# Optimization experiments

Measured on AMD Instinct MI355X. Metric: run time of the kernel, lower is better.

## Reference

```python
import jax, jax.numpy as jnp
import numpy as np

B, S, D, H = 4, 2048, 512, 4
HD = D // H
EPS = 1e-5


def layer_norm(x, gamma, beta):
    mu = jnp.mean(x, axis=-1, keepdims=True)
    var = jnp.mean(jnp.square(x - mu), axis=-1, keepdims=True)
    return (x - mu) * jax.lax.rsqrt(var + EPS) * gamma + beta


def setup_inputs() -> dict:
    key = jax.random.key(0)
    ks = jax.random.split(key, 16)
    s_in = 1.0 / np.sqrt(D)
    s_ex = 1.0 / np.sqrt(2 * D)
    return {
        "input_states": jax.random.normal(ks[0], (B, S, D), jnp.float32),
        "positions": jax.random.normal(ks[1], (B, S, 3), jnp.float32),
        "W_expand": jax.random.uniform(ks[2], (D, 2 * D), jnp.float32, -s_in, s_in),
        "b_expand": jax.random.uniform(ks[3], (2 * D,), jnp.float32, -s_in, s_in),
        "W_squeeze": jax.random.uniform(ks[4], (2 * D, D), jnp.float32, -s_ex, s_ex),
        "b_squeeze": jax.random.uniform(ks[5], (D,), jnp.float32, -s_ex, s_ex),
        "gamma": jnp.ones((D,), jnp.float32),
        "beta": jnp.zeros((D,), jnp.float32),
        "Wq": jax.random.uniform(ks[6], (D, D), jnp.float32, -s_in, s_in),
        "bq": jax.random.uniform(ks[7], (D,), jnp.float32, -s_in, s_in),
        "Wk": jax.random.uniform(ks[8], (D, D), jnp.float32, -s_in, s_in),
        "bk": jax.random.uniform(ks[9], (D,), jnp.float32, -s_in, s_in),
        "Wv": jax.random.uniform(ks[10], (D, D), jnp.float32, -s_in, s_in),
        "bv": jax.random.uniform(ks[11], (D,), jnp.float32, -s_in, s_in),
        "alpha": jnp.float32(0.1),
    }


def reference(input_states, positions, W_expand, b_expand, W_squeeze, b_squeeze,
              gamma, beta, Wq, bq, Wk, bk, Wv, bv, alpha):
    # FFN (expand -> relu -> squeeze) + residual + LayerNorm
    h = jax.nn.relu(input_states @ W_expand + b_expand)
    squeezed = h @ W_squeeze + b_squeeze
    se = layer_norm(input_states + squeezed, gamma, beta)

    # q/k/v projections, split heads: [B,H,S,HD]
    q = (se @ Wq + bq).reshape(B, S, H, HD).transpose(0, 2, 1, 3)
    k = (se @ Wk + bk).reshape(B, S, H, HD).transpose(0, 2, 1, 3)
    v = (se @ Wv + bv).reshape(B, S, H, HD).transpose(0, 2, 1, 3)

    scores = jnp.einsum('bhid,bhjd->bhij', q, k) / np.sqrt(HD)

    # squared pairwise distance bias: ||pi||^2 + ||pj||^2 - 2 pi.pj, broadcast over heads
    sq = jnp.sum(positions * positions, axis=-1)  # [B,S]
    dist2 = sq[:, :, None] + sq[:, None, :] - 2.0 * jnp.einsum('bic,bjc->bij', positions, positions)
    dist2 = jnp.maximum(dist2, 0.0)
    scores = scores - alpha * dist2[:, None, :, :]

    w = jax.nn.softmax(scores, axis=-1)
    ctx = jnp.einsum('bhij,bhjd->bhid', w, v)
    ctx = ctx.transpose(0, 2, 1, 3).reshape(B, S, D)

    # same LayerNorm params reused (self.norm applied twice in original)
    return layer_norm(se + ctx, gamma, beta)
```

## Files before the change

kernel.cpp:

```cpp
#include <hip/hip_runtime.h>

typedef __bf16 bf16_t;
typedef __attribute__((ext_vector_type(8))) __bf16 bf16x8;
typedef __attribute__((ext_vector_type(4))) __bf16 bf16x4;
typedef __attribute__((ext_vector_type(4))) float f32x4;

constexpr int Bc = 4, Sc = 2048, Dc = 512, Hc = 4, HDc = 128;
constexpr int Mrows = Bc * Sc;

__device__ inline void gl2lds(const void* g, void* l) {
  __builtin_amdgcn_global_load_lds(
      (__attribute__((address_space(1))) void*)g,
      (__attribute__((address_space(3))) void*)l, 16, 0, 0);
}

__global__ __launch_bounds__(256) void wt_transpose_k(const float* __restrict__ src,
                                                      bf16_t* __restrict__ dst,
                                                      int K, int N) {
  __shared__ float tile[32][33];
  const int tx = threadIdx.x & 31, ty = threadIdx.x >> 5;
  const int n0 = blockIdx.x * 32, k0 = blockIdx.y * 32;
#pragma unroll
  for (int i = 0; i < 4; i++)
    tile[ty + i * 8][tx] = src[(long)(k0 + ty + i * 8) * N + n0 + tx];
  __syncthreads();
#pragma unroll
  for (int i = 0; i < 4; i++)
    dst[(long)(n0 + ty + i * 8) * K + k0 + tx] = (bf16_t)tile[tx][ty + i * 8];
}

__global__ __launch_bounds__(256) void cvt_k(const float* __restrict__ x,
                                             bf16_t* __restrict__ y) {
  const long i = ((long)blockIdx.x * 256 + threadIdx.x) * 8;
  const float4 a = *(const float4*)(x + i);
  const float4 c = *(const float4*)(x + i + 4);
  bf16x8 o;
  o[0] = (bf16_t)a.x; o[1] = (bf16_t)a.y; o[2] = (bf16_t)a.z; o[3] = (bf16_t)a.w;
  o[4] = (bf16_t)c.x; o[5] = (bf16_t)c.y; o[6] = (bf16_t)c.z; o[7] = (bf16_t)c.w;
  *(bf16x8*)(y + i) = o;
}

__global__ __launch_bounds__(256) void pospack_k(const float* __restrict__ pos,
                                                 float* __restrict__ pos2) {
  const int i = blockIdx.x * 256 + threadIdx.x;
  const float x = pos[(long)i * 3], y = pos[(long)i * 3 + 1], z = pos[(long)i * 3 + 2];
  float4 o; o.x = x; o.y = y; o.z = z; o.w = 0.f;
  *(float4*)(pos2 + (long)i * 4) = o;
}

template <int OMODE>
__global__ __launch_bounds__(256, 2) void gemm128_k(
    const bf16_t* __restrict__ A, const bf16_t* __restrict__ Bt,
    const float* __restrict__ bias0, const float* __restrict__ bias1,
    const float* __restrict__ bias2, void* __restrict__ out0,
    void* __restrict__ out1, void* __restrict__ out2, int N, int K) {
  __shared__ bf16_t As[128 * 32];
  __shared__ bf16_t Bs[128 * 32];
  const int t = threadIdx.x;
  const int n0 = blockIdx.x * 128, m0 = blockIdx.y * 128;
  const int lane = t & 63, wave = t >> 6;
  const int quad = lane >> 4, ln = lane & 15;
  const int wm = wave >> 1, wn = wave & 1;
  const int srow = wave * 16 + (lane >> 2);
  const int scol = (lane & 3) * 8;
  const bf16_t* aseg = A + (long)(m0 + srow) * K + scol;
  const bf16_t* bseg = Bt + (long)(n0 + srow) * K + scol;
  bf16_t* asl = &As[(wave * 16) * 32];
  bf16_t* bsl = &Bs[(wave * 16) * 32];
  f32x4 acc[4][4] = {};
  for (int k0 = 0; k0 < K; k0 += 32) {
#pragma unroll
    for (int i = 0; i < 2; i++) {
      gl2lds(aseg + (long)i * 64 * K + k0, asl + i * 64 * 32);
      gl2lds(bseg + (long)i * 64 * K + k0, bsl + i * 64 * 32);
    }
    __syncthreads();
    bf16x8 af[4], bfr[4];
#pragma unroll
    for (int mt = 0; mt < 4; mt++)
      af[mt] = *(const bf16x8*)&As[(wm * 64 + mt * 16 + ln) * 32 + quad * 8];
#pragma unroll
    for (int nt = 0; nt < 4; nt++)
      bfr[nt] = *(const bf16x8*)&Bs[(wn * 64 + nt * 16 + ln) * 32 + quad * 8];
#pragma unroll
    for (int mt = 0; mt < 4; mt++)
#pragma unroll
      for (int nt = 0; nt < 4; nt++)
        acc[mt][nt] = __builtin_amdgcn_mfma_f32_16x16x32_bf16(af[mt], bfr[nt],
                                                              acc[mt][nt], 0, 0, 0);
    __syncthreads();
  }
#pragma unroll
  for (int nt = 0; nt < 4; nt++) {
    const int gcol = n0 + wn * 64 + nt * 16 + ln;
    if constexpr (OMODE == 0 || OMODE == 1) {
      const float bv = bias0[gcol];
      bf16_t* o = (bf16_t*)out0;
#pragma unroll
      for (int mt = 0; mt < 4; mt++)
#pragma unroll
        for (int r = 0; r < 4; r++) {
          const int grow = m0 + wm * 64 + mt * 16 + quad * 4 + r;
          float vv = acc[mt][nt][r] + bv;
          if constexpr (OMODE == 0) vv = vv > 0.f ? vv : 0.f;
          o[(long)grow * N + gcol] = (bf16_t)vv;
        }
    } else {
      const int which = gcol >> 9, n = gcol & 511;
      const int hh = n >> 7, hd = n & 127;
      const float bv = (which == 0 ? bias0 : which == 1 ? bias1 : bias2)[n];
      bf16_t* o = (bf16_t*)(which == 0 ? out0 : which == 1 ? out1 : out2);
#pragma unroll
      for (int mt = 0; mt < 4; mt++)
#pragma unroll
        for (int r = 0; r < 4; r++) {
          const int grow = m0 + wm * 64 + mt * 16 + quad * 4 + r;
          const int b = grow >> 11, s = grow & 2047;
          const float vv = acc[mt][nt][r] + bv;
          long idx;
          if (which == 2)
            idx = ((long)(b * Hc + hh) * HDc + hd) * Sc + s;
          else
            idx = ((long)(b * Hc + hh) * Sc + s) * HDc + hd;
          o[idx] = (bf16_t)vv;
        }
    }
  }
}

template <int DUAL>
__global__ __launch_bounds__(256) void ln_k(const float* __restrict__ xa,
                                            const bf16_t* __restrict__ xb,
                                            const float* __restrict__ gamma,
                                            const float* __restrict__ beta,
                                            float* __restrict__ out,
                                            bf16_t* __restrict__ outb) {
  const int wave = threadIdx.x >> 6, lane = threadIdx.x & 63;
  const long row = (long)blockIdx.x * 4 + wave;
  const float* a = xa + row * Dc;
  const bf16_t* bp = xb + row * Dc;
  float vv[8];
  float s = 0.f, s2 = 0.f;
#pragma unroll
  for (int i = 0; i < 2; i++) {
    const float4 va = *(const float4*)(a + lane * 4 + i * 256);
    const bf16x4 vb = *(const bf16x4*)(bp + lane * 4 + i * 256);
    const float xs[4] = {va.x, va.y, va.z, va.w};
#pragma unroll
    for (int j = 0; j < 4; j++) {
      const float x = xs[j] + (float)vb[j];
      vv[i * 4 + j] = x;
      s += x;
      s2 += x * x;
    }
  }
#pragma unroll
  for (int off = 1; off < 64; off <<= 1) {
    s += __shfl_xor(s, off, 64);
    s2 += __shfl_xor(s2, off, 64);
  }
  const float mu = s * (1.f / Dc);
  const float var = s2 * (1.f / Dc) - mu * mu;
  const float rstd = rsqrtf(var + 1e-5f);
#pragma unroll
  for (int i = 0; i < 2; i++)
#pragma unroll
    for (int j = 0; j < 4; j++) {
      const int col = lane * 4 + i * 256 + j;
      const float o = (vv[i * 4 + j] - mu) * rstd * gamma[col] + beta[col];
      out[row * Dc + col] = o;
      if constexpr (DUAL) outb[row * Dc + col] = (bf16_t)o;
    }
}

__global__ __launch_bounds__(256, 2) void attn_k(const bf16_t* __restrict__ q,
                                                 const bf16_t* __restrict__ k,
                                                 const bf16_t* __restrict__ v,
                                                 const float* __restrict__ pos2,
                                                 const float* __restrict__ alphap,
                                                 bf16_t* __restrict__ ctx) {
  __shared__ bf16_t Ks[2][64 * 128];
  __shared__ bf16_t Vts[2][128 * 64];
  __shared__ float pk[2][64][4];
  __shared__ bf16_t Ps[4][16][72];
  const int t = threadIdx.x;
  const int qt = blockIdx.x, h = blockIdx.y, b = blockIdx.z;
  const int q0 = qt * 64;
  const int wave = t >> 6, lane = t & 63, quad = lane >> 4, ln = lane & 15;
  const int ln7 = ln & 7;
  const float l2e = 1.4426950408889634f;
  const float scale_l2 = 0.08838834764831845f * l2e;
  const float alpha_l2 = alphap[0] * l2e;
  const bf16_t* kbase = k + (long)(b * Hc + h) * Sc * HDc;
  const bf16_t* vbase = v + (long)(b * Hc + h) * HDc * Sc;

  bf16x8 qf[4];
#pragma unroll
  for (int kc = 0; kc < 4; kc++)
    qf[kc] = *(const bf16x8*)(q + ((long)(b * Hc + h) * Sc + q0 + wave * 16 + ln) * HDc +
                              kc * 32 + quad * 8);
  float pqx[4], pqy[4], pqz[4];
#pragma unroll
  for (int r = 0; r < 4; r++) {
    const float4 p = *(const float4*)(pos2 + ((long)b * Sc + q0 + wave * 16 + quad * 4 + r) * 4);
    pqx[r] = p.x; pqy[r] = p.y; pqz[r] = p.z;
  }

  const int krw = wave * 16 + (lane >> 4);
  const int kg = lane & 15;
  const int vrw = wave * 32 + (lane >> 3);
  const int vg = lane & 7;
  auto stage = [&](int buf, int kt) {
#pragma unroll
    for (int i = 0; i < 4; i++) {
      const int row = krw + i * 4;
      gl2lds(kbase + (long)(kt * 64 + row) * HDc + (kg ^ (row & 7)) * 8,
             &Ks[buf][wave * 2048 + i * 512]);
    }
#pragma unroll
    for (int i = 0; i < 4; i++) {
      const int row = vrw + i * 8;
      gl2lds(vbase + (long)row * Sc + kt * 64 + (vg ^ (row & 7)) * 8,
             &Vts[buf][wave * 2048 + i * 512]);
    }
    if (wave == 0)
      gl2lds(pos2 + ((long)b * Sc + kt * 64) * 4, &pk[buf][0][0]);
  };
  stage(0, 0);

  float rs[4] = {0.f, 0.f, 0.f, 0.f};
  f32x4 acc_o[8] = {};

  for (int kt = 0; kt < Sc / 64; kt++) {
    const int cur = kt & 1;
    __syncthreads();
    if (kt < Sc / 64 - 1) stage(1 - cur, kt + 1);

    f32x4 sacc[4] = {};
#pragma unroll
    for (int kc = 0; kc < 4; kc++)
#pragma unroll
      for (int ct = 0; ct < 4; ct++) {
        const bf16x8 bfv = *(const bf16x8*)&Ks[cur][(ct * 16 + ln) * 128 +
                                                    ((kc * 4 + quad) ^ ln7) * 8];
        sacc[ct] = __builtin_amdgcn_mfma_f32_16x16x32_bf16(qf[kc], bfv, sacc[ct], 0, 0, 0);
      }
#pragma unroll
    for (int ct = 0; ct < 4; ct++) {
      const int kk = ct * 16 + ln;
      const float4 pkv = *(const float4*)&pk[cur][kk][0];
#pragma unroll
      for (int r = 0; r < 4; r++) {
        const float dx = pqx[r] - pkv.x, dy = pqy[r] - pkv.y, dz = pqz[r] - pkv.z;
        const float d2 = dx * dx + dy * dy + dz * dz;
        const float p = __builtin_amdgcn_exp2f(sacc[ct][r] * scale_l2 - alpha_l2 * d2);
        rs[r] += p;
        Ps[wave][quad * 4 + r][kk] = (bf16_t)p;
      }
    }
#pragma unroll
    for (int s2 = 0; s2 < 2; s2++) {
      const bf16x8 pf = *(const bf16x8*)&Ps[wave][ln][s2 * 32 + quad * 8];
#pragma unroll
      for (int nt = 0; nt < 8; nt++) {
        const bf16x8 vf = *(const bf16x8*)&Vts[cur][(nt * 16 + ln) * 64 +
                                                    ((s2 * 4 + quad) ^ ln7) * 8];
        acc_o[nt] = __builtin_amdgcn_mfma_f32_16x16x32_bf16(pf, vf, acc_o[nt], 0, 0, 0);
      }
    }
  }

#pragma unroll
  for (int off = 1; off < 16; off <<= 1)
#pragma unroll
    for (int r = 0; r < 4; r++) rs[r] += __shfl_xor(rs[r], off, 64);
  float rinv[4];
#pragma unroll
  for (int r = 0; r < 4; r++) rinv[r] = 1.f / rs[r];
#pragma unroll
  for (int nt = 0; nt < 8; nt++)
#pragma unroll
    for (int r = 0; r < 4; r++) {
      const int qrow = wave * 16 + quad * 4 + r;
      ctx[((long)b * Sc + q0 + qrow) * Dc + h * HDc + nt * 16 + ln] =
          (bf16_t)(acc_o[nt][r] * rinv[r]);
    }
}

constexpr size_t SE_OFF = 0;
constexpr size_t SQB_OFF = 16777216;
constexpr size_t SEB_OFF = 25165824;
constexpr size_t Q_OFF = 33554432;
constexpr size_t K_OFF = 41943040;
constexpr size_t V_OFF = 50331648;
constexpr size_t XB_OFF = Q_OFF;
constexpr size_t H_OFF = K_OFF;
constexpr size_t POS2_OFF = SEB_OFF;
constexpr size_t WTE_OFF = 58720256;
constexpr size_t WTS_OFF = WTE_OFF + 1048576;
constexpr size_t WTQKV_OFF = WTS_OFF + 1048576;

extern "C" void kernel_launch(void* const* d_in, const int* in_sizes, int n_in,
                              void* d_out, int out_size, void* d_ws, size_t ws_size,
                              hipStream_t stream) {
  const float* X = (const float*)d_in[0];
  const float* pos = (const float*)d_in[1];
  const float* W_expand = (const float*)d_in[2];
  const float* b_expand = (const float*)d_in[3];
  const float* W_squeeze = (const float*)d_in[4];
  const float* b_squeeze = (const float*)d_in[5];
  const float* gamma = (const float*)d_in[6];
  const float* beta = (const float*)d_in[7];
  const float* Wq = (const float*)d_in[8];
  const float* bq = (const float*)d_in[9];
  const float* Wk = (const float*)d_in[10];
  const float* bk = (const float*)d_in[11];
  const float* Wv = (const float*)d_in[12];
  const float* bv = (const float*)d_in[13];
  const float* alphap = (const float*)d_in[14];

  char* ws = (char*)d_ws;
  float* se = (float*)(ws + SE_OFF);
  bf16_t* sqb = (bf16_t*)(ws + SQB_OFF);
  bf16_t* ctxb = (bf16_t*)(ws + SQB_OFF);
  bf16_t* seb = (bf16_t*)(ws + SEB_OFF);
  float* pos2 = (float*)(ws + POS2_OFF);
  bf16_t* qb = (bf16_t*)(ws + Q_OFF);
  bf16_t* kb = (bf16_t*)(ws + K_OFF);
  bf16_t* vb = (bf16_t*)(ws + V_OFF);
  bf16_t* xbb = (bf16_t*)(ws + XB_OFF);
  bf16_t* hb = (bf16_t*)(ws + H_OFF);
  bf16_t* wtE = (bf16_t*)(ws + WTE_OFF);
  bf16_t* wtS = (bf16_t*)(ws + WTS_OFF);
  bf16_t* wtQKV = (bf16_t*)(ws + WTQKV_OFF);

  cvt_k<<<Mrows * Dc / (256 * 8), 256, 0, stream>>>(X, xbb);
  wt_transpose_k<<<dim3(1024 / 32, 512 / 32), 256, 0, stream>>>(W_expand, wtE, 512, 1024);
  wt_transpose_k<<<dim3(512 / 32, 1024 / 32), 256, 0, stream>>>(W_squeeze, wtS, 1024, 512);
  wt_transpose_k<<<dim3(16, 16), 256, 0, stream>>>(Wq, wtQKV, 512, 512);
  wt_transpose_k<<<dim3(16, 16), 256, 0, stream>>>(Wk, wtQKV + 512 * 512, 512, 512);
  wt_transpose_k<<<dim3(16, 16), 256, 0, stream>>>(Wv, wtQKV + 2 * 512 * 512, 512, 512);

  gemm128_k<0><<<dim3(1024 / 128, Mrows / 128), 256, 0, stream>>>(
      xbb, wtE, b_expand, nullptr, nullptr, hb, nullptr, nullptr, 1024, 512);
  gemm128_k<1><<<dim3(512 / 128, Mrows / 128), 256, 0, stream>>>(
      hb, wtS, b_squeeze, nullptr, nullptr, sqb, nullptr, nullptr, 512, 1024);
  ln_k<1><<<Mrows / 4, 256, 0, stream>>>(X, sqb, gamma, beta, se, seb);
  gemm128_k<2><<<dim3(1536 / 128, Mrows / 128), 256, 0, stream>>>(
      seb, wtQKV, bq, bk, bv, qb, kb, vb, 1536, 512);
  pospack_k<<<Mrows / 256, 256, 0, stream>>>(pos, pos2);
  attn_k<<<dim3(Sc / 64, Hc, Bc), 256, 0, stream>>>(qb, kb, vb, pos2, alphap, ctxb);
  ln_k<0><<<Mrows / 4, 256, 0, stream>>>(se, ctxb, gamma, beta, (float*)d_out, nullptr);

  (void)in_sizes; (void)n_in; (void)out_size; (void)ws_size;
}
```

Before: 259.7 us.

## Fuse prep kernels, widen GEMM K-tile, expand distance bias algebraically in attention

Merges the input conversion and five weight transposes into one launch to cut launch overhead. The GEMM now stages a K-tile of 64 instead of 32 per barrier, halving the number of sync rounds, and its occupancy hint rises to 3. Attention precomputes -alpha*||p||^2 per position in pospack and rewrites the distance bias as an FMA chain on pre-scaled query coordinates. It also advances K/V pointers incrementally. The expanded distance form drops the clamp at zero and can lose precision through cancellation.

```diff
diff --git a/kernel.cpp b/kernel.cpp
--- a/kernel.cpp
+++ b/kernel.cpp
@@ -14,12 +14,33 @@
       (__attribute__((address_space(3))) void*)l, 16, 0, 0);
 }
 
-__global__ __launch_bounds__(256) void wt_transpose_k(const float* __restrict__ src,
-                                                      bf16_t* __restrict__ dst,
-                                                      int K, int N) {
+__global__ __launch_bounds__(256) void prep_k(
+    const float* __restrict__ X, bf16_t* __restrict__ xb,
+    const float* __restrict__ We, bf16_t* __restrict__ wtE,
+    const float* __restrict__ Ws, bf16_t* __restrict__ wtS,
+    const float* __restrict__ Wq, const float* __restrict__ Wk,
+    const float* __restrict__ Wv, bf16_t* __restrict__ wtQKV) {
+  const int bid = blockIdx.x;
+  if (bid < 2048) {
+    const long i = ((long)bid * 256 + threadIdx.x) * 8;
+    const float4 a = *(const float4*)(X + i);
+    const float4 c = *(const float4*)(X + i + 4);
+    bf16x8 o;
+    o[0] = (bf16_t)a.x; o[1] = (bf16_t)a.y; o[2] = (bf16_t)a.z; o[3] = (bf16_t)a.w;
+    o[4] = (bf16_t)c.x; o[5] = (bf16_t)c.y; o[6] = (bf16_t)c.z; o[7] = (bf16_t)c.w;
+    *(bf16x8*)(xb + i) = o;
+    return;
+  }
   __shared__ float tile[32][33];
+  const float* src; bf16_t* dst; int K, N, local;
+  if (bid < 2560)      { src = We; dst = wtE; K = 512;  N = 1024; local = bid - 2048; }
+  else if (bid < 3072) { src = Ws; dst = wtS; K = 1024; N = 512;  local = bid - 2560; }
+  else if (bid < 3328) { src = Wq; dst = wtQKV;          K = 512; N = 512; local = bid - 3072; }
+  else if (bid < 3584) { src = Wk; dst = wtQKV + 262144; K = 512; N = 512; local = bid - 3328; }
+  else                 { src = Wv; dst = wtQKV + 524288; K = 512; N = 512; local = bid - 3584; }
+  const int nb = N / 32;
+  const int n0 = (local % nb) * 32, k0 = (local / nb) * 32;
   const int tx = threadIdx.x & 31, ty = threadIdx.x >> 5;
-  const int n0 = blockIdx.x * 32, k0 = blockIdx.y * 32;
 #pragma unroll
   for (int i = 0; i < 4; i++)
     tile[ty + i * 8][tx] = src[(long)(k0 + ty + i * 8) * N + n0 + tx];
@@ -29,65 +50,59 @@
     dst[(long)(n0 + ty + i * 8) * K + k0 + tx] = (bf16_t)tile[tx][ty + i * 8];
 }
 
-__global__ __launch_bounds__(256) void cvt_k(const float* __restrict__ x,
-                                             bf16_t* __restrict__ y) {
-  const long i = ((long)blockIdx.x * 256 + threadIdx.x) * 8;
-  const float4 a = *(const float4*)(x + i);
-  const float4 c = *(const float4*)(x + i + 4);
-  bf16x8 o;
-  o[0] = (bf16_t)a.x; o[1] = (bf16_t)a.y; o[2] = (bf16_t)a.z; o[3] = (bf16_t)a.w;
-  o[4] = (bf16_t)c.x; o[5] = (bf16_t)c.y; o[6] = (bf16_t)c.z; o[7] = (bf16_t)c.w;
-  *(bf16x8*)(y + i) = o;
-}
-
 __global__ __launch_bounds__(256) void pospack_k(const float* __restrict__ pos,
+                                                 const float* __restrict__ alphap,
                                                  float* __restrict__ pos2) {
+  const float aL = alphap[0] * 1.4426950408889634f;
   const int i = blockIdx.x * 256 + threadIdx.x;
   const float x = pos[(long)i * 3], y = pos[(long)i * 3 + 1], z = pos[(long)i * 3 + 2];
-  float4 o; o.x = x; o.y = y; o.z = z; o.w = 0.f;
+  float4 o; o.x = x; o.y = y; o.z = z; o.w = -aL * (x * x + y * y + z * z);
   *(float4*)(pos2 + (long)i * 4) = o;
 }
 
 template <int OMODE>
-__global__ __launch_bounds__(256, 2) void gemm128_k(
+__global__ __launch_bounds__(256, 3) void gemm128_k(
     const bf16_t* __restrict__ A, const bf16_t* __restrict__ Bt,
     const float* __restrict__ bias0, const float* __restrict__ bias1,
     const float* __restrict__ bias2, void* __restrict__ out0,
     void* __restrict__ out1, void* __restrict__ out2, int N, int K) {
-  __shared__ bf16_t As[128 * 32];
-  __shared__ bf16_t Bs[128 * 32];
+  __shared__ bf16_t As[128 * 64];
+  __shared__ bf16_t Bs[128 * 64];
   const int t = threadIdx.x;
   const int n0 = blockIdx.x * 128, m0 = blockIdx.y * 128;
   const int lane = t & 63, wave = t >> 6;
   const int quad = lane >> 4, ln = lane & 15;
   const int wm = wave >> 1, wn = wave & 1;
-  const int srow = wave * 16 + (lane >> 2);
-  const int scol = (lane & 3) * 8;
-  const bf16_t* aseg = A + (long)(m0 + srow) * K + scol;
-  const bf16_t* bseg = Bt + (long)(n0 + srow) * K + scol;
-  bf16_t* asl = &As[(wave * 16) * 32];
-  bf16_t* bsl = &Bs[(wave * 16) * 32];
+  const int srow = wave * 32 + (lane >> 3);
+  const int sgrp = lane & 7;
+  const bf16_t* aseg = A + (long)(m0 + srow) * K + sgrp * 8;
+  const bf16_t* bseg = Bt + (long)(n0 + srow) * K + sgrp * 8;
+  bf16_t* asl = &As[(wave * 32) * 64];
+  bf16_t* bsl = &Bs[(wave * 32) * 64];
   f32x4 acc[4][4] = {};
-  for (int k0 = 0; k0 < K; k0 += 32) {
-#pragma unroll
-    for (int i = 0; i < 2; i++) {
-      gl2lds(aseg + (long)i * 64 * K + k0, asl + i * 64 * 32);
-      gl2lds(bseg + (long)i * 64 * K + k0, bsl + i * 64 * 32);
+  for (int k0 = 0; k0 < K; k0 += 64) {
+#pragma unroll
+    for (int i = 0; i < 4; i++) {
+      gl2lds(aseg + (long)i * 8 * K + k0, asl + i * 8 * 64);
+      gl2lds(bseg + (long)i * 8 * K + k0, bsl + i * 8 * 64);
     }
     __syncthreads();
-    bf16x8 af[4], bfr[4];
-#pragma unroll
-    for (int mt = 0; mt < 4; mt++)
-      af[mt] = *(const bf16x8*)&As[(wm * 64 + mt * 16 + ln) * 32 + quad * 8];
-#pragma unroll
-    for (int nt = 0; nt < 4; nt++)
-      bfr[nt] = *(const bf16x8*)&Bs[(wn * 64 + nt * 16 + ln) * 32 + quad * 8];
-#pragma unroll
-    for (int mt = 0; mt < 4; mt++)
+#pragma unroll
+    for (int kc = 0; kc < 2; kc++) {
+      bf16x8 af[4], bfr[4];
+#pragma unroll
+      for (int mt = 0; mt < 4; mt++)
+        af[mt] = *(const bf16x8*)&As[(wm * 64 + mt * 16 + ln) * 64 + kc * 32 + quad * 8];
 #pragma unroll
       for (int nt = 0; nt < 4; nt++)
-        acc[mt][nt] = __builtin_amdgcn_mfma_f32_16x16x32_bf16(af[mt], bfr[nt],
-                                                              acc[mt][nt], 0, 0, 0);
+        bfr[nt] = *(const bf16x8*)&Bs[(wn * 64 + nt * 16 + ln) * 64 + kc * 32 + quad * 8];
+#pragma unroll
+      for (int mt = 0; mt < 4; mt++)
+#pragma unroll
+        for (int nt = 0; nt < 4; nt++)
+          acc[mt][nt] = __builtin_amdgcn_mfma_f32_16x16x32_bf16(af[mt], bfr[nt],
+                                                                acc[mt][nt], 0, 0, 0);
+    }
     __syncthreads();
   }
 #pragma unroll
@@ -190,7 +205,8 @@
   const int ln7 = ln & 7;
   const float l2e = 1.4426950408889634f;
   const float scale_l2 = 0.08838834764831845f * l2e;
-  const float alpha_l2 = alphap[0] * l2e;
+  const float aL2 = alphap[0] * l2e;
+  const float twoaL = 2.f * aL2;
   const bf16_t* kbase = k + (long)(b * Hc + h) * Sc * HDc;
   const bf16_t* vbase = v + (long)(b * Hc + h) * HDc * Sc;
 
@@ -199,34 +215,35 @@
   for (int kc = 0; kc < 4; kc++)
     qf[kc] = *(const bf16x8*)(q + ((long)(b * Hc + h) * Sc + q0 + wave * 16 + ln) * HDc +
                               kc * 32 + quad * 8);
-  float pqx[4], pqy[4], pqz[4];
+  float pqx[4], pqy[4], pqz[4], pqw[4];
 #pragma unroll
   for (int r = 0; r < 4; r++) {
     const float4 p = *(const float4*)(pos2 + ((long)b * Sc + q0 + wave * 16 + quad * 4 + r) * 4);
-    pqx[r] = p.x; pqy[r] = p.y; pqz[r] = p.z;
+    pqx[r] = twoaL * p.x; pqy[r] = twoaL * p.y; pqz[r] = twoaL * p.z; pqw[r] = p.w;
   }
 
   const int krw = wave * 16 + (lane >> 4);
   const int kg = lane & 15;
   const int vrw = wave * 32 + (lane >> 3);
   const int vg = lane & 7;
-  auto stage = [&](int buf, int kt) {
+  const bf16_t* kcur = kbase;
+  const bf16_t* vcur = vbase;
+  const float* pcur = pos2 + (long)b * Sc * 4;
+  auto stage = [&](int buf) {
 #pragma unroll
     for (int i = 0; i < 4; i++) {
       const int row = krw + i * 4;
-      gl2lds(kbase + (long)(kt * 64 + row) * HDc + (kg ^ (row & 7)) * 8,
-             &Ks[buf][wave * 2048 + i * 512]);
+      gl2lds(kcur + (long)row * HDc + (kg ^ (row & 7)) * 8, &Ks[buf][wave * 2048 + i * 512]);
     }
 #pragma unroll
     for (int i = 0; i < 4; i++) {
       const int row = vrw + i * 8;
-      gl2lds(vbase + (long)row * Sc + kt * 64 + (vg ^ (row & 7)) * 8,
-             &Vts[buf][wave * 2048 + i * 512]);
-    }
-    if (wave == 0)
-      gl2lds(pos2 + ((long)b * Sc + kt * 64) * 4, &pk[buf][0][0]);
+      gl2lds(vcur + (long)row * Sc + (vg ^ (row & 7)) * 8, &Vts[buf][wave * 2048 + i * 512]);
+    }
+    if (wave == 0) gl2lds(pcur, &pk[buf][0][0]);
   };
-  stage(0, 0);
+  stage(0);
+  kcur += 64 * HDc; vcur += 64; pcur += 256;
 
   float rs[4] = {0.f, 0.f, 0.f, 0.f};
   f32x4 acc_o[8] = {};
@@ -234,7 +251,10 @@
   for (int kt = 0; kt < Sc / 64; kt++) {
     const int cur = kt & 1;
     __syncthreads();
-    if (kt < Sc / 64 - 1) stage(1 - cur, kt + 1);
+    if (kt < Sc / 64 - 1) {
+      stage(1 - cur);
+      kcur += 64 * HDc; vcur += 64; pcur += 256;
+    }
 
     f32x4 sacc[4] = {};
 #pragma unroll
@@ -251,9 +271,11 @@
       const float4 pkv = *(const float4*)&pk[cur][kk][0];
 #pragma unroll
       for (int r = 0; r < 4; r++) {
-        const float dx = pqx[r] - pkv.x, dy = pqy[r] - pkv.y, dz = pqz[r] - pkv.z;
-        const float d2 = dx * dx + dy * dy + dz * dz;
-        const float p = __builtin_amdgcn_exp2f(sacc[ct][r] * scale_l2 - alpha_l2 * d2);
+        float base = pqw[r] + pkv.w;
+        base = __builtin_fmaf(pqx[r], pkv.x, base);
+        base = __builtin_fmaf(pqy[r], pkv.y, base);
+        base = __builtin_fmaf(pqz[r], pkv.z, base);
+        const float p = __builtin_amdgcn_exp2f(__builtin_fmaf(sacc[ct][r], scale_l2, base));
         rs[r] += p;
         Ps[wave][quad * 4 + r][kk] = (bf16_t)p;
       }
@@ -334,12 +356,8 @@
   bf16_t* wtS = (bf16_t*)(ws + WTS_OFF);
   bf16_t* wtQKV = (bf16_t*)(ws + WTQKV_OFF);
 
-  cvt_k<<<Mrows * Dc / (256 * 8), 256, 0, stream>>>(X, xbb);
-  wt_transpose_k<<<dim3(1024 / 32, 512 / 32), 256, 0, stream>>>(W_expand, wtE, 512, 1024);
-  wt_transpose_k<<<dim3(512 / 32, 1024 / 32), 256, 0, stream>>>(W_squeeze, wtS, 1024, 512);
-  wt_transpose_k<<<dim3(16, 16), 256, 0, stream>>>(Wq, wtQKV, 512, 512);
-  wt_transpose_k<<<dim3(16, 16), 256, 0, stream>>>(Wk, wtQKV + 512 * 512, 512, 512);
-  wt_transpose_k<<<dim3(16, 16), 256, 0, stream>>>(Wv, wtQKV + 2 * 512 * 512, 512, 512);
+  prep_k<<<3840, 256, 0, stream>>>(X, xbb, W_expand, wtE, W_squeeze, wtS,
+                                   Wq, Wk, Wv, wtQKV);
 
   gemm128_k<0><<<dim3(1024 / 128, Mrows / 128), 256, 0, stream>>>(
       xbb, wtE, b_expand, nullptr, nullptr, hb, nullptr, nullptr, 1024, 512);
@@ -348,7 +366,7 @@
   ln_k<1><<<Mrows / 4, 256, 0, stream>>>(X, sqb, gamma, beta, se, seb);
   gemm128_k<2><<<dim3(1536 / 128, Mrows / 128), 256, 0, stream>>>(
       seb, wtQKV, bq, bk, bv, qb, kb, vb, 1536, 512);
-  pospack_k<<<Mrows / 256, 256, 0, stream>>>(pos, pos2);
+  pospack_k<<<Mrows / 256, 256, 0, stream>>>(pos, alphap, pos2);
   attn_k<<<dim3(Sc / 64, Hc, Bc), 256, 0, stream>>>(qb, kb, vb, pos2, alphap, ctxb);
   ln_k<0><<<Mrows / 4, 256, 0, stream>>>(se, ctxb, gamma, beta, (float*)d_out, nullptr);
 
```

Measured after the change: 243.4 us. 6.3% less time.
